# Kernel optimization log

Measured on AMD Instinct MI355X. Metric: run time of the kernel, lower is better.

Reference implementation:

```python
import jax, jax.numpy as jnp
import numpy as np

N_NODES = 50000
N_EDGES = 600000
IN_FEATS = 128
OUT_FEATS = 128


def setup_inputs() -> dict:
    key = jax.random.key(0)
    k1, k2, k3, k4, k5 = jax.random.split(key, 5)
    feature = jax.random.normal(k1, (N_NODES, IN_FEATS), dtype=jnp.float32)
    src = jax.random.randint(k2, (N_EDGES,), 0, N_NODES, dtype=jnp.int64)
    dst = jax.random.randint(k3, (N_EDGES,), 0, N_NODES, dtype=jnp.int64)
    # nn.Linear params (PyTorch stores weight as [out, in])
    bound = 1.0 / np.sqrt(IN_FEATS)
    W = jax.random.uniform(k4, (OUT_FEATS, IN_FEATS), dtype=jnp.float32, minval=-bound, maxval=bound)
    b = jax.random.uniform(k5, (OUT_FEATS,), dtype=jnp.float32, minval=-bound, maxval=bound)
    return {"feature": feature, "W": W, "b": b, "src": src, "dst": dst}


def reference(feature, W, b, src, dst):
    # copy_src + sum: aggregate src features onto dst nodes (SpMM)
    agg = jax.ops.segment_sum(feature[src], dst, num_segments=N_NODES)  # [N, in]
    # linear + tanh
    return jnp.tanh(agg @ W.T + b)  # [N, out]
```

## Files before the change

### kernel.cpp

```cpp
#include <hip/hip_runtime.h>
#include <hip/hip_fp16.h>
#include <math.h>

constexpr int kNodes = 50000;
constexpr int kEdges = 600000;
constexpr int kF     = 128;
constexpr int kNPB   = 64;
constexpr int kCap   = 48;
constexpr int kStr   = 136;
constexpr int kCPad  = 16;

constexpr int kGemmB = (kNodes + kNPB - 1) / kNPB;
constexpr int kFillB = (kEdges + 255) / 256;

constexpr size_t kOffWt     = 0;
constexpr size_t kOffCursor = 65536;
constexpr size_t kOffBucket = 65536 + 3200000;
constexpr size_t kOffGpk    = kOffBucket + (size_t)kNodes * kCap * 4;
constexpr size_t kWsNeeded  = kOffGpk + (size_t)kNodes * kF * 2;

typedef _Float16 v8h __attribute__((ext_vector_type(8)));
typedef float    v4f __attribute__((ext_vector_type(4)));

static __device__ __forceinline__ unsigned int packh2(float a, float b) {
    __half2 h = __floats2half2_rn(a, b);
    return *reinterpret_cast<unsigned int*>(&h);
}

__global__ __launch_bounds__(256) void prep0(const float* __restrict__ W,
                                             float* __restrict__ Wt,
                                             int* __restrict__ cursor) {
    int gid = blockIdx.x * 256 + threadIdx.x;
    if (gid < kF * kF) {
        int k = gid >> 7;
        int o = gid & (kF - 1);
        Wt[gid] = W[o * kF + k];
    }
    if (gid < kNodes) {
        uint4 z = {0, 0, 0, 0};
        uint4* c4 = reinterpret_cast<uint4*>(cursor) + gid * 4;
        c4[0] = z; c4[1] = z; c4[2] = z; c4[3] = z;
    }
}

__global__ __launch_bounds__(256, 3) void gemm_fill(const float* __restrict__ F,
                                                    const float* __restrict__ Wg,
                                                    const int* __restrict__ src,
                                                    const int* __restrict__ dst,
                                                    int* __restrict__ cursor,
                                                    int* __restrict__ bucket,
                                                    uint2* __restrict__ Gpk2) {
    __shared__ __align__(16) unsigned short sW[kF * kStr];
    __shared__ __align__(16) unsigned short sF[kNPB * kStr];

    const int t = threadIdx.x;

    if (blockIdx.x < kFillB) {
        int e = blockIdx.x * 256 + t;
        if (e < kEdges) {
            int d = dst[e];
            int p = atomicAdd(&cursor[d * kCPad], 1);
            if (p < kCap) bucket[d * kCap + p] = src[e];
        }
        return;
    }

    const int n0 = (blockIdx.x - kFillB) * kNPB;
    const int rows = min(kNPB, kNodes - n0);

    for (int idx = t; idx < kF * 16; idx += 256) {
        int o = idx >> 4, c = idx & 15;
        const float4* wp = reinterpret_cast<const float4*>(Wg + o * kF + c * 8);
        float4 w0 = wp[0], w1 = wp[1];
        uint4 pk;
        pk.x = packh2(w0.x, w0.y);
        pk.y = packh2(w0.z, w0.w);
        pk.z = packh2(w1.x, w1.y);
        pk.w = packh2(w1.z, w1.w);
        *reinterpret_cast<uint4*>(&sW[o * kStr + c * 8]) = pk;
    }
    for (int idx = t; idx < rows * 16; idx += 256) {
        int n = idx >> 4, c = idx & 15;
        const float4* fp = reinterpret_cast<const float4*>(F + (size_t)(n0 + n) * kF + c * 8);
        float4 f0 = fp[0], f1 = fp[1];
        uint4 pk;
        pk.x = packh2(f0.x, f0.y);
        pk.y = packh2(f0.z, f0.w);
        pk.z = packh2(f1.x, f1.y);
        pk.w = packh2(f1.z, f1.w);
        *reinterpret_cast<uint4*>(&sF[n * kStr + c * 8]) = pk;
    }
    __syncthreads();

    const int wv   = t >> 6;
    const int lane = t & 63;
    const int m    = lane & 15;
    const int quad = lane >> 4;

    v8h bfrag[4];
#pragma unroll
    for (int kc = 0; kc < 4; ++kc)
        bfrag[kc] = *reinterpret_cast<const v8h*>(&sF[(wv * 16 + m) * kStr + kc * 32 + quad * 8]);

    const int node = n0 + wv * 16 + m;
#pragma unroll
    for (int ot = 0; ot < 8; ++ot) {
        v4f acc = {0.0f, 0.0f, 0.0f, 0.0f};
#pragma unroll
        for (int kc = 0; kc < 4; ++kc) {
            v8h afrag = *reinterpret_cast<const v8h*>(&sW[(ot * 16 + m) * kStr + kc * 32 + quad * 8]);
            acc = __builtin_amdgcn_mfma_f32_16x16x32_f16(afrag, bfrag[kc], acc, 0, 0, 0);
        }
        if (node < kNodes) {
            uint2 p;
            p.x = packh2(acc[0], acc[1]);
            p.y = packh2(acc[2], acc[3]);
            Gpk2[(size_t)node * 32 + ot * 4 + quad] = p;
        }
    }
}

__global__ __launch_bounds__(256) void gather_tanh(const uint4* __restrict__ Gpk4,
                                                   const int* __restrict__ bucket,
                                                   const int* __restrict__ cursor,
                                                   const float* __restrict__ bias,
                                                   float* __restrict__ out) {
    const int wave = (blockIdx.x * 256 + threadIdx.x) >> 6;
    const int lane = threadIdx.x & 63;
    if (wave >= kNodes) return;
    const int grp = lane >> 4;
    const int sub = lane & 15;

    const int deg = min(cursor[wave * kCPad], kCap);
    const int base = wave * kCap;

    int eid = (lane < deg) ? bucket[base + lane] : 0;

    float acc[8];
#pragma unroll
    for (int i = 0; i < 8; ++i) acc[i] = 0.0f;

    const int iters = (deg + 3) >> 2;
#pragma unroll 2
    for (int i = 0; i < iters; ++i) {
        const int j = grp + 4 * i;
        const bool valid = (j < deg);
        int s = __shfl(eid, valid ? j : 0);
        if (valid) {
            uint4 u = Gpk4[(size_t)s * 16 + sub];
            const __half2* hp = reinterpret_cast<const __half2*>(&u);
#pragma unroll
            for (int q = 0; q < 4; ++q) {
                float2 f = __half22float2(hp[q]);
                acc[2 * q]     += f.x;
                acc[2 * q + 1] += f.y;
            }
        }
    }

#pragma unroll
    for (int i = 0; i < 8; ++i) {
        acc[i] += __shfl_xor(acc[i], 16);
        acc[i] += __shfl_xor(acc[i], 32);
    }

    if (grp == 0) {
        float4 b0 = *reinterpret_cast<const float4*>(bias + sub * 8);
        float4 b1 = *reinterpret_cast<const float4*>(bias + sub * 8 + 4);
        float4 r0, r1;
        r0.x = 1.0f - 2.0f / (__expf(2.0f * (acc[0] + b0.x)) + 1.0f);
        r0.y = 1.0f - 2.0f / (__expf(2.0f * (acc[1] + b0.y)) + 1.0f);
        r0.z = 1.0f - 2.0f / (__expf(2.0f * (acc[2] + b0.z)) + 1.0f);
        r0.w = 1.0f - 2.0f / (__expf(2.0f * (acc[3] + b0.w)) + 1.0f);
        r1.x = 1.0f - 2.0f / (__expf(2.0f * (acc[4] + b1.x)) + 1.0f);
        r1.y = 1.0f - 2.0f / (__expf(2.0f * (acc[5] + b1.y)) + 1.0f);
        r1.z = 1.0f - 2.0f / (__expf(2.0f * (acc[6] + b1.z)) + 1.0f);
        r1.w = 1.0f - 2.0f / (__expf(2.0f * (acc[7] + b1.w)) + 1.0f);
        float4* dst = reinterpret_cast<float4*>(out + (size_t)wave * kF + sub * 8);
        dst[0] = r0;
        dst[1] = r1;
    }
}

__global__ __launch_bounds__(256) void scatter_add(const float* __restrict__ feature,
                                                   const int* __restrict__ src,
                                                   const int* __restrict__ dst,
                                                   float* __restrict__ agg) {
    int gid = blockIdx.x * 256 + threadIdx.x;
    int e = gid >> 5;
    int c = (gid & 31) << 2;
    float4 v = *reinterpret_cast<const float4*>(feature + (size_t)src[e] * kF + c);
    float* p = agg + (size_t)dst[e] * kF + c;
    atomicAdd(p + 0, v.x);
    atomicAdd(p + 1, v.y);
    atomicAdd(p + 2, v.z);
    atomicAdd(p + 3, v.w);
}

__global__ __launch_bounds__(256, 4) void linear_tanh(float* __restrict__ inout,
                                                      const float* __restrict__ Wt,
                                                      const float* __restrict__ bias) {
    __shared__ float sAgg[kNPB * kF];
    __shared__ float sB[kF];
    const int t  = threadIdx.x;
    const int n0 = blockIdx.x * kNPB;
    if (t < kF) sB[t] = bias[t];
    const int rows = min(kNPB, kNodes - n0);
    for (int i = t * 4; i < rows * kF; i += 256 * 4)
        *reinterpret_cast<float4*>(&sAgg[i]) =
            *reinterpret_cast<const float4*>(inout + (size_t)n0 * kF + i);
    __syncthreads();
    const int tn = t >> 5, to = t & 31, nb = tn * 8;
    float acc[8][4];
#pragma unroll
    for (int n = 0; n < 8; ++n)
#pragma unroll
        for (int j = 0; j < 4; ++j) acc[n][j] = 0.0f;
    for (int k = 0; k < kF; k += 4) {
        float4 wt[4];
#pragma unroll
        for (int i = 0; i < 4; ++i)
            wt[i] = *reinterpret_cast<const float4*>(Wt + (k + i) * kF + to * 4);
#pragma unroll
        for (int n = 0; n < 8; ++n) {
            float4 av = *reinterpret_cast<const float4*>(&sAgg[(nb + n) * kF + k]);
#pragma unroll
            for (int j = 0; j < 4; ++j) {
                const float* w0 = reinterpret_cast<const float*>(&wt[0]);
                const float* w1 = reinterpret_cast<const float*>(&wt[1]);
                const float* w2 = reinterpret_cast<const float*>(&wt[2]);
                const float* w3 = reinterpret_cast<const float*>(&wt[3]);
                acc[n][j] += av.x * w0[j] + av.y * w1[j] + av.z * w2[j] + av.w * w3[j];
            }
        }
    }
#pragma unroll
    for (int n = 0; n < 8; ++n) {
        int node = n0 + nb + n;
        if (node < kNodes) {
            float4 r;
            r.x = 1.0f - 2.0f / (__expf(2.0f * (acc[n][0] + sB[to * 4 + 0])) + 1.0f);
            r.y = 1.0f - 2.0f / (__expf(2.0f * (acc[n][1] + sB[to * 4 + 1])) + 1.0f);
            r.z = 1.0f - 2.0f / (__expf(2.0f * (acc[n][2] + sB[to * 4 + 2])) + 1.0f);
            r.w = 1.0f - 2.0f / (__expf(2.0f * (acc[n][3] + sB[to * 4 + 3])) + 1.0f);
            *reinterpret_cast<float4*>(inout + (size_t)node * kF + to * 4) = r;
        }
    }
}

extern "C" void kernel_launch(void* const* d_in, const int* in_sizes, int n_in,
                              void* d_out, int out_size, void* d_ws, size_t ws_size,
                              hipStream_t stream) {
    const float* feature = (const float*)d_in[0];
    const float* W       = (const float*)d_in[1];
    const float* b       = (const float*)d_in[2];
    const int*   src     = (const int*)d_in[3];
    const int*   dst     = (const int*)d_in[4];
    float* out = (float*)d_out;

    char* ws = (char*)d_ws;
    float* Wt     = (float*)(ws + kOffWt);
    int*   cursor = (int*)(ws + kOffCursor);
    int*   bucket = (int*)(ws + kOffBucket);
    uint2* Gpk2   = (uint2*)(ws + kOffGpk);

    if (ws_size >= kWsNeeded) {
        prep0<<<(kNodes + 255) / 256, 256, 0, stream>>>(W, Wt, cursor);
        gemm_fill<<<kFillB + kGemmB, 256, 0, stream>>>(
            feature, W, src, dst, cursor, bucket, Gpk2);
        gather_tanh<<<(kNodes + 3) / 4, 256, 0, stream>>>(
            (const uint4*)Gpk2, bucket, cursor, b, out);
    } else {
        prep0<<<(kNodes + 255) / 256, 256, 0, stream>>>(W, Wt, cursor);
        hipMemsetAsync(out, 0, (size_t)kNodes * kF * sizeof(float), stream);
        scatter_add<<<(kEdges * 32) / 256, 256, 0, stream>>>(feature, src, dst, out);
        linear_tanh<<<(kNodes + kNPB - 1) / kNPB, 256, 0, stream>>>(out, Wt, b);
    }
}
```

Baseline: 162.8 us.

## Split fused gemm/fill kernel and load feature fragments directly from global

Splits the combined edge-bucket-fill and GEMM kernel into two separate launches, so fill blocks no longer carry the GEMM's shared-memory footprint. The GEMM kernel now converts each feature row straight into fp16 MFMA B-fragments in registers and drops the sF shared-memory staging buffer. This lowers LDS use and raises the occupancy hint to 4. The cost is an extra kernel launch, and the fill and GEMM blocks can no longer overlap within a single grid.

```diff
diff --git a/kernel.cpp b/kernel.cpp
--- a/kernel.cpp
+++ b/kernel.cpp
@@ -43,30 +43,49 @@
     }
 }
 
-__global__ __launch_bounds__(256, 3) void gemm_fill(const float* __restrict__ F,
+__global__ __launch_bounds__(256) void bucket_fill(const int* __restrict__ src,
+                                                   const int* __restrict__ dst,
+                                                   int* __restrict__ cursor,
+                                                   int* __restrict__ bucket) {
+    int e = blockIdx.x * 256 + threadIdx.x;
+    if (e < kEdges) {
+        int d = dst[e];
+        int p = atomicAdd(&cursor[d * kCPad], 1);
+        if (p < kCap) bucket[d * kCap + p] = src[e];
+    }
+}
+
+__global__ __launch_bounds__(256, 4) void gemm_mfma(const float* __restrict__ F,
                                                     const float* __restrict__ Wg,
-                                                    const int* __restrict__ src,
-                                                    const int* __restrict__ dst,
-                                                    int* __restrict__ cursor,
-                                                    int* __restrict__ bucket,
                                                     uint2* __restrict__ Gpk2) {
     __shared__ __align__(16) unsigned short sW[kF * kStr];
-    __shared__ __align__(16) unsigned short sF[kNPB * kStr];
 
     const int t = threadIdx.x;
-
-    if (blockIdx.x < kFillB) {
-        int e = blockIdx.x * 256 + t;
-        if (e < kEdges) {
-            int d = dst[e];
-            int p = atomicAdd(&cursor[d * kCPad], 1);
-            if (p < kCap) bucket[d * kCap + p] = src[e];
-        }
-        return;
-    }
-
-    const int n0 = (blockIdx.x - kFillB) * kNPB;
-    const int rows = min(kNPB, kNodes - n0);
+    const int n0 = blockIdx.x * kNPB;
+
+    const int wv   = t >> 6;
+    const int lane = t & 63;
+    const int m    = lane & 15;
+    const int quad = lane >> 4;
+
+    const int node = n0 + wv * 16 + m;
+    const int nrow = min(node, kNodes - 1);
+
+    const float* frow = F + (size_t)nrow * kF;
+    v8h bfrag[4];
+#pragma unroll
+    for (int kc = 0; kc < 4; ++kc) {
+        const float4* fp = reinterpret_cast<const float4*>(frow + kc * 32 + quad * 8);
+        float4 f0 = fp[0], f1 = fp[1];
+        uint4 pk;
+        pk.x = packh2(f0.x, f0.y);
+        pk.y = packh2(f0.z, f0.w);
+        pk.z = packh2(f1.x, f1.y);
+        pk.w = packh2(f1.z, f1.w);
+        union { uint4 u; v8h h; } cvt;
+        cvt.u = pk;
+        bfrag[kc] = cvt.h;
+    }
 
     for (int idx = t; idx < kF * 16; idx += 256) {
         int o = idx >> 4, c = idx & 15;
@@ -79,30 +98,8 @@
         pk.w = packh2(w1.z, w1.w);
         *reinterpret_cast<uint4*>(&sW[o * kStr + c * 8]) = pk;
     }
-    for (int idx = t; idx < rows * 16; idx += 256) {
-        int n = idx >> 4, c = idx & 15;
-        const float4* fp = reinterpret_cast<const float4*>(F + (size_t)(n0 + n) * kF + c * 8);
-        float4 f0 = fp[0], f1 = fp[1];
-        uint4 pk;
-        pk.x = packh2(f0.x, f0.y);
-        pk.y = packh2(f0.z, f0.w);
-        pk.z = packh2(f1.x, f1.y);
-        pk.w = packh2(f1.z, f1.w);
-        *reinterpret_cast<uint4*>(&sF[n * kStr + c * 8]) = pk;
-    }
     __syncthreads();
 
-    const int wv   = t >> 6;
-    const int lane = t & 63;
-    const int m    = lane & 15;
-    const int quad = lane >> 4;
-
-    v8h bfrag[4];
-#pragma unroll
-    for (int kc = 0; kc < 4; ++kc)
-        bfrag[kc] = *reinterpret_cast<const v8h*>(&sF[(wv * 16 + m) * kStr + kc * 32 + quad * 8]);
-
-    const int node = n0 + wv * 16 + m;
 #pragma unroll
     for (int ot = 0; ot < 8; ++ot) {
         v4f acc = {0.0f, 0.0f, 0.0f, 0.0f};
@@ -266,8 +263,8 @@
 
     if (ws_size >= kWsNeeded) {
         prep0<<<(kNodes + 255) / 256, 256, 0, stream>>>(W, Wt, cursor);
-        gemm_fill<<<kFillB + kGemmB, 256, 0, stream>>>(
-            feature, W, src, dst, cursor, bucket, Gpk2);
+        bucket_fill<<<kFillB, 256, 0, stream>>>(src, dst, cursor, bucket);
+        gemm_mfma<<<kGemmB, 256, 0, stream>>>(feature, W, Gpk2);
         gather_tanh<<<(kNodes + 3) / 4, 256, 0, stream>>>(
             (const uint4*)Gpk2, bucket, cursor, b, out);
     } else {
```

Result: faster. 150.5 us (-7.6%).
